# Performance work log

Measured on AMD Instinct MI355X. Metric: run time of the kernel, lower is better.

The kernel has to match this reference:

```python
import jax, jax.numpy as jnp
import numpy as np

H = 64
L = 3
NG = 1024
# node types: 0 user, 1 card, 2 transaction, 3 merchant, 4 location, 5 device
N_NODES = [100000, 150000, 500000, 20000, 5000, 50000]
N_TX = N_NODES[2]
FEAT_DIMS = [8, 6, 12, 6, 5, 5]
NAMES = ["user", "card", "transaction", "merchant", "location", "device"]
# relation r -> (src_type, dst_type); order matches the HeteroConv dict:
# owns, made, at, in, using, followed_by, owned_by, made_with, receives, has, used_in, preceded
REL = [(0, 1), (1, 2), (2, 3), (2, 4), (2, 5), (2, 2), (1, 0), (2, 1), (3, 2), (4, 2), (5, 2), (2, 2)]
E_CNT = [150000, 500000, 500000, 500000, 500000, 500000, 150000, 500000, 500000, 500000, 500000, 500000]


def gat_conv(x_src, x_dst, src, dst, W, a_s, a_d, b, n_dst):
    # PyG GATConv, heads=1, shared src/dst linear (int in_channels), no self-loops (bipartite hetero)
    xs = x_src @ W  # [Ns, H]
    xd = x_dst @ W  # [Nd, H]
    e = jax.nn.leaky_relu((xs @ a_s)[src] + (xd @ a_d)[dst], 0.2)  # [E]
    m = jax.ops.segment_max(e, dst, num_segments=n_dst)
    m = jnp.where(jnp.isfinite(m), m, 0.0)
    p = jnp.exp(e - m[dst])
    s = jax.ops.segment_sum(p, dst, num_segments=n_dst)
    alpha = p / (s[dst] + 1e-16)
    out = jax.ops.segment_sum(alpha[:, None] * xs[src], dst, num_segments=n_dst)
    return out + b


def setup_inputs():
    key = jax.random.key(0)
    ks = iter(jax.random.split(key, 80))
    inp = {}
    for n, d, nm in zip(N_NODES, FEAT_DIMS, NAMES):
        inp["x_" + nm] = jax.random.normal(next(ks), (n, d), jnp.float32)
    for d, nm in zip(FEAT_DIMS, NAMES):
        inp["emb_" + nm + "_W"] = (jax.random.normal(next(ks), (d, H), jnp.float32) / np.sqrt(d)).astype(jnp.float32)
        inp["emb_" + nm + "_b"] = jnp.zeros((H,), jnp.float32)
    inp["gat_W"] = (jax.random.normal(next(ks), (L, 12, H, H), jnp.float32) / np.sqrt(H)).astype(jnp.float32)
    inp["gat_a_src"] = jax.random.normal(next(ks), (L, 12, H), jnp.float32) * 0.1
    inp["gat_a_dst"] = jax.random.normal(next(ks), (L, 12, H), jnp.float32) * 0.1
    inp["gat_b"] = jnp.zeros((L, 12, H), jnp.float32)
    inp["pool_W"] = (jax.random.normal(next(ks), (2 * H, H), jnp.float32) / np.sqrt(2 * H)).astype(jnp.float32)
    inp["pool_b"] = jnp.zeros((H,), jnp.float32)
    inp["cls_W1"] = (jax.random.normal(next(ks), (H, H), jnp.float32) / np.sqrt(H)).astype(jnp.float32)
    inp["cls_b1"] = jnp.zeros((H,), jnp.float32)
    inp["cls_W2"] = (jax.random.normal(next(ks), (H, 1), jnp.float32) / np.sqrt(H)).astype(jnp.float32)
    inp["cls_b2"] = jnp.zeros((1,), jnp.float32)
    for r, (s, d) in enumerate(REL):
        inp[f"e{r}_src"] = jax.random.randint(next(ks), (E_CNT[r],), 0, N_NODES[s])
        inp[f"e{r}_dst"] = jax.random.randint(next(ks), (E_CNT[r],), 0, N_NODES[d])
    inp["batch"] = jnp.sort(jax.random.randint(next(ks), (N_TX,), 0, NG))
    return inp


def reference(x_user, x_card, x_transaction, x_merchant, x_location, x_device,
              emb_user_W, emb_user_b, emb_card_W, emb_card_b,
              emb_transaction_W, emb_transaction_b, emb_merchant_W, emb_merchant_b,
              emb_location_W, emb_location_b, emb_device_W, emb_device_b,
              gat_W, gat_a_src, gat_a_dst, gat_b,
              pool_W, pool_b, cls_W1, cls_b1, cls_W2, cls_b2,
              e0_src, e0_dst, e1_src, e1_dst, e2_src, e2_dst, e3_src, e3_dst,
              e4_src, e4_dst, e5_src, e5_dst, e6_src, e6_dst, e7_src, e7_dst,
              e8_src, e8_dst, e9_src, e9_dst, e10_src, e10_dst, e11_src, e11_dst,
              batch):
    edges = [(e0_src, e0_dst), (e1_src, e1_dst), (e2_src, e2_dst), (e3_src, e3_dst),
             (e4_src, e4_dst), (e5_src, e5_dst), (e6_src, e6_dst), (e7_src, e7_dst),
             (e8_src, e8_dst), (e9_src, e9_dst), (e10_src, e10_dst), (e11_src, e11_dst)]
    x = [x_user @ emb_user_W + emb_user_b,
         x_card @ emb_card_W + emb_card_b,
         x_transaction @ emb_transaction_W + emb_transaction_b,
         x_merchant @ emb_merchant_W + emb_merchant_b,
         x_location @ emb_location_W + emb_location_b,
         x_device @ emb_device_W + emb_device_b]
    for l in range(L):
        agg = [jnp.zeros((n, H), x[0].dtype) for n in N_NODES]
        for r, (s, d) in enumerate(REL):  # HeteroConv default aggr='sum'
            agg[d] = agg[d] + gat_conv(x[s], x[d], edges[r][0], edges[r][1],
                                       gat_W[l, r], gat_a_src[l, r], gat_a_dst[l, r],
                                       gat_b[l, r], N_NODES[d])
        x = [jax.nn.relu(a) for a in agg]  # dropout(p=0.2) is identity in eval mode
    tx = x[2]
    cnt = jax.ops.segment_sum(jnp.ones((N_TX,), tx.dtype), batch, num_segments=NG)
    mean_pool = jax.ops.segment_sum(tx, batch, num_segments=NG) / jnp.maximum(cnt, 1.0)[:, None]
    max_pool = jax.ops.segment_max(tx, batch, num_segments=NG)
    max_pool = jnp.where(jnp.isfinite(max_pool), max_pool, 0.0)
    pooled = jnp.concatenate([mean_pool, max_pool], axis=1) @ pool_W + pool_b
    h = jax.nn.relu(tx @ cls_W1 + cls_b1)
    fraud_scores = jax.nn.sigmoid(h @ cls_W2 + cls_b2)
    return fraud_scores, pooled
```

## Files before the change

### kernel.cpp

```cpp
#include <hip/hip_runtime.h>
#include <hip/hip_bf16.h>

typedef unsigned int u32;
typedef unsigned short u16;
typedef _Float16 f16;
typedef float f32x4 __attribute__((ext_vector_type(4)));
typedef short bf16x8 __attribute__((ext_vector_type(8)));

#define CDIV(a,b) (((a)+(b)-1)/(b))

__device__ __forceinline__ float bf2f(u32 h){ return __uint_as_float(h<<16); }
__device__ __forceinline__ u16 f2bf(float f){
  u32 u=__float_as_uint(f);
  return (u16)((u + 0x7fffu + ((u>>16)&1u))>>16);
}
__device__ __forceinline__ void unpack8(const u16* p, float* xr){
  uint4 v=*(const uint4*)p;
  xr[0]=bf2f(v.x&0xffffu); xr[1]=bf2f(v.x>>16);
  xr[2]=bf2f(v.y&0xffffu); xr[3]=bf2f(v.y>>16);
  xr[4]=bf2f(v.z&0xffffu); xr[5]=bf2f(v.z>>16);
  xr[6]=bf2f(v.w&0xffffu); xr[7]=bf2f(v.w>>16);
}
__device__ __forceinline__ int iclamp(int i, int n){
  unsigned u=(unsigned)i; return (u>=(unsigned)n)?0:i;
}

struct EdgeTab {
  const int* dst[12];
  const int* src[12];
  int seo[13];
  int rpo[13];
  int nd[12];
  int ns[12];
};

struct GTab {
  int nn[6]; int xo[6];
  int rst[12];
  int aso[12], ado[12], rpo[12], seo[12];
  int tord[6]; int bofs[7];
  int abofs[7];
  int nrel[6], rel[6][6];
  int nrole[6]; int rwv[6][12]; int rofs[6][12];
  int dszb;
};

__global__ void kdiag(float* out, int n, float v){
  int i=blockIdx.x*blockDim.x+threadIdx.x;
  if(i<n) out[i]=(i==0)?v:0.f;
}
__global__ void kzeroi(int* p, int n){
  int i=blockIdx.x*blockDim.x+threadIdx.x;
  if(i<n) p[i]=0;
}
__global__ void kbsum(const float* __restrict__ gb, float* __restrict__ bsum){
  int l=blockIdx.x/6, t=blockIdx.x%6, j=threadIdx.x;
  const int rd[12]={1,2,3,4,5,2,0,1,2,2,2,2};
  float a=0.f;
  #pragma unroll
  for(int r=0;r<12;++r) if(rd[r]==t) a += gb[(l*12+r)*64 + j];
  bsum[(l*6+t)*64 + j]=a;
}
__global__ void kwconv(const float* __restrict__ gw, u16* __restrict__ wt, int total){
  int o=blockIdx.x*blockDim.x+threadIdx.x;
  if(o>=total) return;
  int m=o>>12, rem=o&4095, j=rem>>6, k=rem&63;
  wt[o]=f2bf(gw[(m<<12)+(k<<6)+j]);
}
__global__ void kwv(const float* __restrict__ gw, const float* __restrict__ gas,
                    const float* __restrict__ gad, float* __restrict__ wv){
  int m=blockIdx.x;
  int lr=m>>1, role=m&1;
  int k=threadIdx.x;
  const float* a=(role?gad:gas)+(size_t)lr*64;
  const float* W=gw+(size_t)lr*4096;
  float acc=0.f;
  for(int j=0;j<64;++j) acc += W[k*64+j]*a[j];
  wv[(size_t)m*64+k]=acc;
}

__global__ void khistAll(EdgeTab et, int* __restrict__ RP, int Etot){
  int i=blockIdx.x*blockDim.x+threadIdx.x;
  if(i>=Etot) return;
  int r=0;
  #pragma unroll
  for(int k=1;k<12;++k) r += (i>=et.seo[k]) ? 1 : 0;
  int e=i-et.seo[r];
  int d=iclamp(et.dst[r][e], et.nd[r]);
  atomicAdd(RP+et.rpo[r]+d,1);
}
__global__ void kscan1(const int* __restrict__ hist, int* __restrict__ rp, int* __restrict__ bsum, int N){
  __shared__ int lds[256];
  __shared__ int pref[256];
  int b=blockIdx.x, t=threadIdx.x;
  int base=b*4096+t*16;
  int v[16]; int s=0;
  #pragma unroll
  for(int k=0;k<16;++k){ int idx=base+k; v[k]=(idx<N)?hist[idx]:0; s+=v[k]; }
  lds[t]=s; __syncthreads();
  if(t==0){ int run=0; for(int i=0;i<256;++i){ pref[i]=run; run+=lds[i]; } bsum[b]=run; }
  __syncthreads();
  int run=pref[t];
  #pragma unroll
  for(int k=0;k<16;++k){ int idx=base+k; if(idx<N) rp[idx]=run; run+=v[k]; }
}
__global__ void kscan2b(int* bsum, int nb){
  __shared__ int lds[256], pref[256], tot;
  int t=threadIdx.x;
  int v[4]; int s=0;
  #pragma unroll
  for(int k=0;k<4;++k){ int idx=t*4+k; v[k]=(idx<nb)?bsum[idx]:0; s+=v[k]; }
  lds[t]=s; __syncthreads();
  if(t==0){ int run=0; for(int i=0;i<256;++i){ pref[i]=run; run+=lds[i]; } tot=run; }
  __syncthreads();
  int run=pref[t];
  #pragma unroll
  for(int k=0;k<4;++k){ int idx=t*4+k; if(idx<nb){ int x=v[k]; bsum[idx]=run; run+=x; } }
  if(t==0) bsum[nb]=tot;
}
__global__ void kscan3(int* __restrict__ rp, const int* __restrict__ bsum, int N){
  int i=blockIdx.x*blockDim.x+threadIdx.x;
  if(i<N) rp[i]+=bsum[i>>12];
}
__global__ void kscatterAll(EdgeTab et, int* __restrict__ RP, int* __restrict__ SRCS, int Etot){
  int i=blockIdx.x*blockDim.x+threadIdx.x;
  if(i>=Etot) return;
  int r=0;
  #pragma unroll
  for(int k=1;k<12;++k) r += (i>=et.seo[k]) ? 1 : 0;
  int e=i-et.seo[r];
  int d=iclamp(et.dst[r][e], et.nd[r]);
  int pos=atomicAdd(RP+et.rpo[r]+d,1);
  SRCS[pos]=iclamp(et.src[r][e], et.ns[r]);
}

template<int D>
__global__ void kemb(const float* __restrict__ xin, const float* __restrict__ W,
                     const float* __restrict__ b, u16* __restrict__ xout, int N){
  int n=blockIdx.x*blockDim.x+threadIdx.x;
  if(n>=N) return;
  float xr[D];
  #pragma unroll
  for(int k=0;k<D;++k) xr[k]=xin[(long)n*D+k];
  u16* orow=xout+(long)n*64;
  for(int j0=0;j0<64;j0+=8){
    float acc[8];
    #pragma unroll
    for(int jj=0;jj<8;++jj){
      float a=b[j0+jj];
      #pragma unroll
      for(int k=0;k<D;++k) a += xr[k]*W[k*64+j0+jj];
      acc[jj]=a;
    }
    uint4 pk;
    pk.x=(u32)f2bf(acc[0])|((u32)f2bf(acc[1])<<16);
    pk.y=(u32)f2bf(acc[2])|((u32)f2bf(acc[3])<<16);
    pk.z=(u32)f2bf(acc[4])|((u32)f2bf(acc[5])<<16);
    pk.w=(u32)f2bf(acc[6])|((u32)f2bf(acc[7])<<16);
    *(uint4*)(orow+j0)=pk;
  }
}

__global__ void kalphaM(const u16* __restrict__ X, const float* __restrict__ WVl,
                        f16* __restrict__ AA, GTab tab){
  __shared__ float wv[12*64];
  int b=blockIdx.x, tid=threadIdx.x;
  int ti=0;
  #pragma unroll
  for(int k=1;k<6;++k) ti += (b>=tab.abofs[k]) ? 1 : 0;
  int t=tab.tord[ti];
  int nr=tab.nrole[t];
  for(int i=tid;i<nr*64;i+=256){
    int ro=i>>6, j=i&63;
    wv[i]=WVl[tab.rwv[t][ro]*64+j];
  }
  __syncthreads();
  int nid=(b-tab.abofs[ti])*256+tid;
  if(nid>=tab.nn[t]) return;
  const u16* row=X+((long)tab.xo[t]+nid)*64;
  float xr[64];
  #pragma unroll
  for(int j=0;j<64;j+=8) unpack8(row+j,xr+j);
  for(int ro=0;ro<nr;++ro){
    float acc=0.f;
    #pragma unroll
    for(int k=0;k<64;++k) acc += xr[k]*wv[ro*64+k];
    AA[tab.rofs[t][ro]+nid]=(f16)acc;
  }
}

#define LZ 0
#define LW 8192
__global__ void kfusedM2(const u16* __restrict__ Xc, u16* __restrict__ Xn,
                         const u16* __restrict__ WTl, const f16* __restrict__ AA,
                         const int* __restrict__ RP, const int* __restrict__ SRCS,
                         const float* __restrict__ BSl, GTab tab){
  __shared__ char L[16384];
  int tid=threadIdx.x;
  int b=blockIdx.x;
  int ti=0;
  #pragma unroll
  for(int k=1;k<6;++k) ti += (b>=tab.bofs[k]) ? 1 : 0;
  int t=tab.tord[ti];
  int d0=(b-tab.bofs[ti])*64;
  int Nt=tab.nn[t];
  int nid=tid>>2, q=tid&3;
  int d=d0+nid;

  f32x4 acc[4];
  #pragma unroll
  for(int ct=0;ct<4;++ct){ acc[ct][0]=0.f; acc[ct][1]=0.f; acc[ct][2]=0.f; acc[ct][3]=0.f; }

  int nrel=tab.nrel[t];
  for(int ri=0;ri<nrel;++ri){
    int r=tab.rel[t][ri];
    __syncthreads();
    {
      const uint4* s4=(const uint4*)(WTl+(size_t)r*4096);
      uint4 v0=s4[tid*2], v1=s4[tid*2+1];
      int b0=tid*32, j=b0>>7;
      *(uint4*)(L+LW+((b0   )^((j&7)<<4)))=v0;
      *(uint4*)(L+LW+((b0+16)^((j&7)<<4)))=v1;
    }
    float z[16];
    #pragma unroll
    for(int k=0;k<16;++k) z[k]=0.f;
    float sden=0.f;
    if(d<Nt){
      int b1=RP[tab.rpo[r]+d];
      int b0e= d? RP[tab.rpo[r]+d-1] : tab.seo[r];
      float adv=(float)AA[tab.dszb+tab.ado[r]+d];
      const u16* xbase=Xc+(long)tab.xo[tab.rst[r]]*64;
      const f16* asp=AA+tab.aso[r];
      float m=-3.4e38f;
      for(int e=b0e;e<b1;++e){
        float ev=(float)asp[SRCS[e]]+adv;
        ev = ev>=0.f?ev:0.2f*ev;
        m=fmaxf(m,ev);
      }
      int e=b0e;
      for(; e+1<b1; e+=2){
        int sr0=SRCS[e], sr1=SRCS[e+1];
        float ev0=(float)asp[sr0]+adv; ev0 = ev0>=0.f?ev0:0.2f*ev0;
        float ev1=(float)asp[sr1]+adv; ev1 = ev1>=0.f?ev1:0.2f*ev1;
        float p0=__expf(ev0-m), p1=__expf(ev1-m);
        uint4 v0=*(const uint4*)(xbase+(long)sr0*64+q*16);
        uint4 v1=*(const uint4*)(xbase+(long)sr1*64+q*16);
        sden+=p0+p1;
        float xr[8];
        unpack8((const u16*)&v0,xr);
        #pragma unroll
        for(int k=0;k<8;++k) z[k]+=p0*xr[k];
        { uint2 hi; hi.x=v0.z; hi.y=v0.w;
          float xh[4];
          xh[0]=bf2f(hi.x&0xffffu); xh[1]=bf2f(hi.x>>16);
          xh[2]=bf2f(hi.y&0xffffu); xh[3]=bf2f(hi.y>>16);
          (void)xh;
        }
        unpack8((const u16*)&v1,xr);
        #pragma unroll
        for(int k=0;k<8;++k) z[8+k]+=0.f;
        (void)p1;
      }
      #pragma unroll
      for(int k=0;k<16;++k) z[k]=0.f;
      sden=0.f;
      for(e=b0e; e+1<b1; e+=2){
        int sr0=SRCS[e], sr1=SRCS[e+1];
        float ev0=(float)asp[sr0]+adv; ev0 = ev0>=0.f?ev0:0.2f*ev0;
        float ev1=(float)asp[sr1]+adv; ev1 = ev1>=0.f?ev1:0.2f*ev1;
        float p0=__expf(ev0-m), p1=__expf(ev1-m);
        const u16* rw0=xbase+(long)sr0*64+q*16;
        const u16* rw1=xbase+(long)sr1*64+q*16;
        uint4 a0=*(const uint4*)rw0;
        uint4 a1=*(const uint4*)(rw0+8);
        uint4 c0=*(const uint4*)rw1;
        uint4 c1=*(const uint4*)(rw1+8);
        sden+=p0+p1;
        float xr[8];
        unpack8((const u16*)&a0,xr);
        #pragma unroll
        for(int k=0;k<8;++k) z[k]+=p0*xr[k];
        unpack8((const u16*)&a1,xr);
        #pragma unroll
        for(int k=0;k<8;++k) z[8+k]+=p0*xr[k];
        unpack8((const u16*)&c0,xr);
        #pragma unroll
        for(int k=0;k<8;++k) z[k]+=p1*xr[k];
        unpack8((const u16*)&c1,xr);
        #pragma unroll
        for(int k=0;k<8;++k) z[8+k]+=p1*xr[k];
      }
      if(e<b1){
        int sr0=SRCS[e];
        float ev0=(float)asp[sr0]+adv; ev0 = ev0>=0.f?ev0:0.2f*ev0;
        float p0=__expf(ev0-m);
        const u16* rw0=xbase+(long)sr0*64+q*16;
        uint4 a0=*(const uint4*)rw0;
        uint4 a1=*(const uint4*)(rw0+8);
        sden+=p0;
        float xr[8];
        unpack8((const u16*)&a0,xr);
        #pragma unroll
        for(int k=0;k<8;++k) z[k]+=p0*xr[k];
        unpack8((const u16*)&a1,xr);
        #pragma unroll
        for(int k=0;k<8;++k) z[8+k]+=p0*xr[k];
      }
    }
    float inv=1.f/(sden+1e-16f);
    {
      uint4 p0,p1;
      p0.x=(u32)f2bf(z[0]*inv) |((u32)f2bf(z[1]*inv)<<16);
      p0.y=(u32)f2bf(z[2]*inv) |((u32)f2bf(z[3]*inv)<<16);
      p0.z=(u32)f2bf(z[4]*inv) |((u32)f2bf(z[5]*inv)<<16);
      p0.w=(u32)f2bf(z[6]*inv) |((u32)f2bf(z[7]*inv)<<16);
      p1.x=(u32)f2bf(z[8]*inv) |((u32)f2bf(z[9]*inv)<<16);
      p1.y=(u32)f2bf(z[10]*inv)|((u32)f2bf(z[11]*inv)<<16);
      p1.z=(u32)f2bf(z[12]*inv)|((u32)f2bf(z[13]*inv)<<16);
      p1.w=(u32)f2bf(z[14]*inv)|((u32)f2bf(z[15]*inv)<<16);
      int zb=nid*128+q*32;
      *(uint4*)(L+LZ+((zb   )^((nid&7)<<4)))=p0;
      *(uint4*)(L+LZ+((zb+16)^((nid&7)<<4)))=p1;
    }
    __syncthreads();
    {
      int w=tid>>6, l=tid&63;
      int nt=w*16;
      int arow=nt+(l&15);
      int kb=(l>>4)*8;
      #pragma unroll
      for(int ks=0;ks<64;ks+=32){
        int ab=arow*128+(ks+kb)*2;
        uint4 av=*(uint4*)(L+LZ+(ab^((arow&7)<<4)));
        bf16x8 af=*(bf16x8*)&av;
        #pragma unroll
        for(int ct=0;ct<4;++ct){
          int jrow=ct*16+(l&15);
          int bb=jrow*128+(ks+kb)*2;
          uint4 bv=*(uint4*)(L+LW+(bb^((jrow&7)<<4)));
          bf16x8 bfr=*(bf16x8*)&bv;
          acc[ct]=__builtin_amdgcn_mfma_f32_16x16x32_bf16(af,bfr,acc[ct],0,0,0);
        }
      }
    }
  }
  __syncthreads();
  {
    int w=tid>>6, l=tid&63;
    int nt=w*16;
    #pragma unroll
    for(int ct=0;ct<4;++ct){
      #pragma unroll
      for(int r4=0;r4<4;++r4){
        int crow=nt+(l>>4)*4+r4;
        int ccol=ct*16+(l&15);
        int cb=crow*256+ccol*4;
        *(float*)(L+(cb^((crow&7)<<4)))=acc[ct][r4];
      }
    }
  }
  __syncthreads();
  {
    int nn=tid>>2, cq=tid&3;
    if(d0+nn<Nt){
      float cv[16];
      #pragma unroll
      for(int p=0;p<4;++p){
        int cb=nn*256+cq*64+p*16;
        uint4 v=*(uint4*)(L+(cb^((nn&7)<<4)));
        const float* f=(const float*)&v;
        cv[p*4+0]=f[0]; cv[p*4+1]=f[1]; cv[p*4+2]=f[2]; cv[p*4+3]=f[3];
      }
      const float* bs=BSl+t*64+cq*16;
      u32 wd[8];
      #pragma unroll
      for(int i=0;i<8;++i){
        float lo=fmaxf(cv[2*i]  +bs[2*i],  0.f);
        float hi=fmaxf(cv[2*i+1]+bs[2*i+1],0.f);
        wd[i]=(u32)f2bf(lo)|((u32)f2bf(hi)<<16);
      }
      u16* orow=Xn+((long)tab.xo[t]+d0+nn)*64+cq*16;
      uint4 s0; s0.x=wd[0]; s0.y=wd[1]; s0.z=wd[2]; s0.w=wd[3];
      uint4 s1; s1.x=wd[4]; s1.y=wd[5]; s1.z=wd[6]; s1.w=wd[7];
      *(uint4*)orow=s0;
      *(uint4*)(orow+8)=s1;
    }
  }
}

__global__ void kcls(const u16* __restrict__ tx, const float* __restrict__ W1,
                     const float* __restrict__ b1, const float* __restrict__ W2,
                     const float* __restrict__ b2, float* __restrict__ out, int N){
  int n=blockIdx.x*blockDim.x+threadIdx.x;
  if(n>=N) return;
  const u16* row=tx+(long)n*64;
  float xr[64];
  #pragma unroll
  for(int j=0;j<64;j+=8) unpack8(row+j,xr+j);
  float acc2=0.f;
  for(int j=0;j<64;++j){
    float a=b1[j];
    #pragma unroll
    for(int k=0;k<64;++k) a += xr[k]*W1[k*64+j];
    a=fmaxf(a,0.f);
    acc2 += a*W2[j];
  }
  float zv=acc2+b2[0];
  out[n]=1.f/(1.f+__expf(-zv));
}

__global__ void kgrp(const int* __restrict__ batch, int* __restrict__ grp, int N){
  int g=blockIdx.x*blockDim.x+threadIdx.x;
  if(g>1024) return;
  if(g==1024){ grp[1024]=N; return; }
  int lo=0, hi=N;
  while(lo<hi){ int mid=(lo+hi)>>1; if(batch[mid]<g) lo=mid+1; else hi=mid; }
  grp[g]=lo;
}
__global__ void kpoolf(const u16* __restrict__ tx, const int* __restrict__ grp,
                       const float* __restrict__ pW, const float* __restrict__ pb,
                       float* __restrict__ out){
  __shared__ float S[256], M[256], V[128];
  int g=blockIdx.x, t=threadIdx.x, w=t>>6, j=t&63;
  int n0=grp[g], n1=grp[g+1];
  float s=0.f, m=-3.4e38f;
  for(int n=n0+w; n<n1; n+=4){
    float v=bf2f(tx[(long)n*64+j]);
    s+=v; m=fmaxf(m,v);
  }
  S[t]=s; M[t]=m; __syncthreads();
  if(t<64){
    float ss=S[t]+S[t+64]+S[t+128]+S[t+192];
    float mm=fmaxf(fmaxf(M[t],M[t+64]),fmaxf(M[t+128],M[t+192]));
    int cnt=n1-n0;
    V[t]=ss/fmaxf((float)cnt,1.f);
    V[64+t]=(cnt>0)?mm:0.f;
  }
  __syncthreads();
  if(t<64){
    float acc=pb[t];
    for(int k=0;k<128;++k) acc+=V[k]*pW[k*64+t];
    out[(long)g*64+t]=acc;
  }
}

extern "C" void kernel_launch(void* const* d_in, const int* in_sizes, int n_in,
                              void* d_out, int out_size, void* d_ws, size_t ws_size,
                              hipStream_t stream){
  const int   NN[6]={100000,150000,500000,20000,5000,50000};
  const long  XO[6]={0,100000,250000,750000,770000,775000};
  const int   RS[12]={0,1,2,2,2,2,1,2,3,4,5,2};
  const int   RD[12]={1,2,3,4,5,2,0,1,2,2,2,2};
  const int   EC[12]={150000,500000,500000,500000,500000,500000,150000,500000,500000,500000,500000,500000};

  const float* xin[6];  for(int t=0;t<6;++t) xin[t]=(const float*)d_in[t];
  const float* embW[6]; const float* embB[6];
  for(int t=0;t<6;++t){ embW[t]=(const float*)d_in[6+2*t]; embB[t]=(const float*)d_in[7+2*t]; }
  const float* gatW =(const float*)d_in[18];
  const float* gatAs=(const float*)d_in[19];
  const float* gatAd=(const float*)d_in[20];
  const float* gatB =(const float*)d_in[21];
  const float* poolW=(const float*)d_in[22];
  const float* poolB=(const float*)d_in[23];
  const float* W1=(const float*)d_in[24];
  const float* b1=(const float*)d_in[25];
  const float* W2=(const float*)d_in[26];
  const float* b2=(const float*)d_in[27];
  const int* esrc[12]; const int* edst[12];
  for(int r=0;r<12;++r){ esrc[r]=(const int*)d_in[28+2*r]; edst[r]=(const int*)d_in[29+2*r]; }
  const int* batch=(const int*)d_in[52];
  float* out=(float*)d_out;
  (void)in_sizes; (void)n_in;

  EdgeTab et;
  GTab tab;
  int rpo=0, seo=0, asz=0, dsz=0;
  for(int r=0;r<12;++r){
    et.dst[r]=edst[r]; et.src[r]=esrc[r];
    et.seo[r]=seo; et.rpo[r]=rpo;
    et.nd[r]=NN[RD[r]]; et.ns[r]=NN[RS[r]];
    tab.rst[r]=RS[r];
    tab.seo[r]=seo; tab.rpo[r]=rpo;
    tab.aso[r]=asz; tab.ado[r]=dsz;
    seo+=EC[r]; rpo+=NN[RD[r]]+1;
    asz+=NN[RS[r]]; dsz+=NN[RD[r]];
  }
  et.seo[12]=seo; et.rpo[12]=rpo;
  const int Etot=seo;
  const int RPtot=rpo;
  tab.dszb=asz;
  for(int t=0;t<6;++t){ tab.nn[t]=NN[t]; tab.xo[t]=(int)XO[t]; }
  const int TORD[6]={4,3,5,2,1,0};
  int bo=0, abo=0;
  for(int i=0;i<6;++i){
    int t=TORD[i];
    tab.tord[i]=t;
    tab.bofs[i]=bo;   bo+=CDIV(NN[t],64);
    tab.abofs[i]=abo; abo+=CDIV(NN[t],256);
  }
  tab.bofs[6]=bo; tab.abofs[6]=abo;
  for(int t=0;t<6;++t){ tab.nrel[t]=0; tab.nrole[t]=0; }
  for(int r=0;r<12;++r){
    int dt=RD[r];
    tab.rel[dt][tab.nrel[dt]++]=r;
    int st=RS[r];
    tab.rwv[st][tab.nrole[st]]=r*2+0;   tab.rofs[st][tab.nrole[st]++]=tab.aso[r];
    tab.rwv[dt][tab.nrole[dt]]=r*2+1;   tab.rofs[dt][tab.nrole[dt]++]=asz+tab.ado[r];
  }

  char* w=(char*)d_ws;
  size_t off=0;
  auto take=[&](size_t bytes)->void*{
    void* p=w+off; off+=(bytes+(size_t)255)&~(size_t)255; return p;
  };
  u16*   X1   =(u16*)  take(105600000);
  u16*   X2   =(u16*)  take(105600000);
  int*   RP   =(int*)  take((size_t)RPtot*4);
  int*   SRCS =(int*)  take((size_t)Etot*4);
  int*   BS   =(int*)  take(4096);
  f16*   AA   =(f16*)  take((size_t)(asz+dsz)*2);
  float* WV   =(float*)take(72*64*4);
  float* BSUM =(float*)take(4608);
  int*   GRP  =(int*)  take(4104);
  u16*   WT   =(u16*)  take(294912);
  size_t need=off;

  const int B=256;

  if(ws_size<need){
    kdiag<<<CDIV(out_size,B),B,0,stream>>>(out,out_size,(float)(ws_size>>20));
    return;
  }

  int nbs=CDIV(RPtot,4096);
  kzeroi<<<CDIV(RPtot,B),B,0,stream>>>(RP,RPtot);
  khistAll<<<CDIV(Etot,B),B,0,stream>>>(et,RP,Etot);
  kscan1<<<nbs,256,0,stream>>>(RP,RP,BS,RPtot);
  kscan2b<<<1,256,0,stream>>>(BS,nbs);
  kscan3<<<CDIV(RPtot,B),B,0,stream>>>(RP,BS,RPtot);
  kscatterAll<<<CDIV(Etot,B),B,0,stream>>>(et,RP,SRCS,Etot);

  kwconv<<<CDIV(147456,B),B,0,stream>>>(gatW,WT,147456);
  kwv<<<72,64,0,stream>>>(gatW,gatAs,gatAd,WV);
  kbsum<<<18,64,0,stream>>>(gatB,BSUM);

  kemb< 8><<<CDIV(NN[0],B),B,0,stream>>>(xin[0],embW[0],embB[0],X1+XO[0]*64,NN[0]);
  kemb< 6><<<CDIV(NN[1],B),B,0,stream>>>(xin[1],embW[1],embB[1],X1+XO[1]*64,NN[1]);
  kemb<12><<<CDIV(NN[2],B),B,0,stream>>>(xin[2],embW[2],embB[2],X1+XO[2]*64,NN[2]);
  kemb< 6><<<CDIV(NN[3],B),B,0,stream>>>(xin[3],embW[3],embB[3],X1+XO[3]*64,NN[3]);
  kemb< 5><<<CDIV(NN[4],B),B,0,stream>>>(xin[4],embW[4],embB[4],X1+XO[4]*64,NN[4]);
  kemb< 5><<<CDIV(NN[5],B),B,0,stream>>>(xin[5],embW[5],embB[5],X1+XO[5]*64,NN[5]);

  u16* Xc=X1; u16* Xn=X2;
  for(int l=0;l<3;++l){
    kalphaM<<<abo,256,0,stream>>>(Xc,WV+(size_t)l*1536,AA,tab);
    kfusedM2<<<bo,256,0,stream>>>(Xc,Xn,WT+(size_t)l*49152,AA,RP,SRCS,BSUM+(size_t)l*384,tab);
    u16* tmp=Xc; Xc=Xn; Xn=tmp;
  }

  kcls<<<CDIV(NN[2],B),B,0,stream>>>(Xc+XO[2]*64,W1,b1,W2,b2,out,NN[2]);

  kgrp<<<CDIV(1025,B),B,0,stream>>>(batch,GRP,NN[2]);
  kpoolf<<<1024,256,0,stream>>>(Xc+XO[2]*64,GRP,poolW,poolB,out+500000);
}
```

Baseline: 2.491 ms.

## Chunk CSR build, fuse layer-0 attention logits into embedding, drop dead loop

Splits the destination histogram and scatter into 8 passes, each over a range of row-pointer indices, so the atomics in one pass stay within a smaller region and may get better cache locality. The cost is reading all edges 8 times per pass. Folds the layer-0 attention logit computation into the embedding kernel and skips the separate kalphaM launch for layer 0. Removes a leftover first aggregation loop in the fused conv kernel whose results were thrown away, which wasted gathers and exps.

```diff
diff --git a/kernel.cpp b/kernel.cpp
--- a/kernel.cpp
+++ b/kernel.cpp
@@ -79,15 +79,15 @@
   wv[(size_t)m*64+k]=acc;
 }
 
-__global__ void khistAll(EdgeTab et, int* __restrict__ RP, int Etot){
+__global__ void khistC(EdgeTab et, int* __restrict__ RP, int Etot, int c0, int c1){
   int i=blockIdx.x*blockDim.x+threadIdx.x;
   if(i>=Etot) return;
   int r=0;
   #pragma unroll
   for(int k=1;k<12;++k) r += (i>=et.seo[k]) ? 1 : 0;
   int e=i-et.seo[r];
-  int d=iclamp(et.dst[r][e], et.nd[r]);
-  atomicAdd(RP+et.rpo[r]+d,1);
+  int rpidx=et.rpo[r]+iclamp(et.dst[r][e], et.nd[r]);
+  if(rpidx>=c0 && rpidx<c1) atomicAdd(RP+rpidx,1);
 }
 __global__ void kscan1(const int* __restrict__ hist, int* __restrict__ rp, int* __restrict__ bsum, int N){
   __shared__ int lds[256];
@@ -122,42 +122,55 @@
   int i=blockIdx.x*blockDim.x+threadIdx.x;
   if(i<N) rp[i]+=bsum[i>>12];
 }
-__global__ void kscatterAll(EdgeTab et, int* __restrict__ RP, int* __restrict__ SRCS, int Etot){
+__global__ void kscatterC(EdgeTab et, int* __restrict__ RP, int* __restrict__ SRCS,
+                          int Etot, int c0, int c1){
   int i=blockIdx.x*blockDim.x+threadIdx.x;
   if(i>=Etot) return;
   int r=0;
   #pragma unroll
   for(int k=1;k<12;++k) r += (i>=et.seo[k]) ? 1 : 0;
   int e=i-et.seo[r];
-  int d=iclamp(et.dst[r][e], et.nd[r]);
-  int pos=atomicAdd(RP+et.rpo[r]+d,1);
-  SRCS[pos]=iclamp(et.src[r][e], et.ns[r]);
+  int rpidx=et.rpo[r]+iclamp(et.dst[r][e], et.nd[r]);
+  if(rpidx>=c0 && rpidx<c1){
+    int pos=atomicAdd(RP+rpidx,1);
+    SRCS[pos]=iclamp(et.src[r][e], et.ns[r]);
+  }
 }
 
 template<int D>
 __global__ void kemb(const float* __restrict__ xin, const float* __restrict__ W,
-                     const float* __restrict__ b, u16* __restrict__ xout, int N){
+                     const float* __restrict__ b, u16* __restrict__ xout, int N,
+                     const float* __restrict__ WV0, f16* __restrict__ AA, GTab tab, int t){
   int n=blockIdx.x*blockDim.x+threadIdx.x;
   if(n>=N) return;
   float xr[D];
   #pragma unroll
   for(int k=0;k<D;++k) xr[k]=xin[(long)n*D+k];
+  float o[64];
   u16* orow=xout+(long)n*64;
+  #pragma unroll
   for(int j0=0;j0<64;j0+=8){
-    float acc[8];
     #pragma unroll
     for(int jj=0;jj<8;++jj){
       float a=b[j0+jj];
       #pragma unroll
       for(int k=0;k<D;++k) a += xr[k]*W[k*64+j0+jj];
-      acc[jj]=a;
+      o[j0+jj]=a;
     }
     uint4 pk;
-    pk.x=(u32)f2bf(acc[0])|((u32)f2bf(acc[1])<<16);
-    pk.y=(u32)f2bf(acc[2])|((u32)f2bf(acc[3])<<16);
-    pk.z=(u32)f2bf(acc[4])|((u32)f2bf(acc[5])<<16);
-    pk.w=(u32)f2bf(acc[6])|((u32)f2bf(acc[7])<<16);
+    pk.x=(u32)f2bf(o[j0+0])|((u32)f2bf(o[j0+1])<<16);
+    pk.y=(u32)f2bf(o[j0+2])|((u32)f2bf(o[j0+3])<<16);
+    pk.z=(u32)f2bf(o[j0+4])|((u32)f2bf(o[j0+5])<<16);
+    pk.w=(u32)f2bf(o[j0+6])|((u32)f2bf(o[j0+7])<<16);
     *(uint4*)(orow+j0)=pk;
+  }
+  int nr=tab.nrole[t];
+  for(int ro=0;ro<nr;++ro){
+    const float* wv=WV0+(size_t)tab.rwv[t][ro]*64;
+    float acc=0.f;
+    #pragma unroll
+    for(int k=0;k<64;++k) acc += o[k]*wv[k];
+    AA[tab.rofs[t][ro]+n]=(f16)acc;
   }
 }
 
@@ -240,32 +253,6 @@
       }
       int e=b0e;
       for(; e+1<b1; e+=2){
-        int sr0=SRCS[e], sr1=SRCS[e+1];
-        float ev0=(float)asp[sr0]+adv; ev0 = ev0>=0.f?ev0:0.2f*ev0;
-        float ev1=(float)asp[sr1]+adv; ev1 = ev1>=0.f?ev1:0.2f*ev1;
-        float p0=__expf(ev0-m), p1=__expf(ev1-m);
-        uint4 v0=*(const uint4*)(xbase+(long)sr0*64+q*16);
-        uint4 v1=*(const uint4*)(xbase+(long)sr1*64+q*16);
-        sden+=p0+p1;
-        float xr[8];
-        unpack8((const u16*)&v0,xr);
-        #pragma unroll
-        for(int k=0;k<8;++k) z[k]+=p0*xr[k];
-        { uint2 hi; hi.x=v0.z; hi.y=v0.w;
-          float xh[4];
-          xh[0]=bf2f(hi.x&0xffffu); xh[1]=bf2f(hi.x>>16);
-          xh[2]=bf2f(hi.y&0xffffu); xh[3]=bf2f(hi.y>>16);
-          (void)xh;
-        }
-        unpack8((const u16*)&v1,xr);
-        #pragma unroll
-        for(int k=0;k<8;++k) z[8+k]+=0.f;
-        (void)p1;
-      }
-      #pragma unroll
-      for(int k=0;k<16;++k) z[k]=0.f;
-      sden=0.f;
-      for(e=b0e; e+1<b1; e+=2){
         int sr0=SRCS[e], sr1=SRCS[e+1];
         float ev0=(float)asp[sr0]+adv; ev0 = ev0>=0.f?ev0:0.2f*ev0;
         float ev1=(float)asp[sr1]+adv; ev1 = ev1>=0.f?ev1:0.2f*ev1;
@@ -533,29 +520,38 @@
     return;
   }
 
+  kwconv<<<CDIV(147456,B),B,0,stream>>>(gatW,WT,147456);
+  kwv<<<72,64,0,stream>>>(gatW,gatAs,gatAd,WV);
+  kbsum<<<18,64,0,stream>>>(gatB,BSUM);
+
+  const int NCH=8;
+  int CS=CDIV(RPtot,NCH);
+  kzeroi<<<CDIV(RPtot,B),B,0,stream>>>(RP,RPtot);
+  for(int c=0;c<NCH;++c){
+    int c0=c*CS, c1=min(RPtot,c0+CS);
+    khistC<<<CDIV(Etot,B),B,0,stream>>>(et,RP,Etot,c0,c1);
+  }
   int nbs=CDIV(RPtot,4096);
-  kzeroi<<<CDIV(RPtot,B),B,0,stream>>>(RP,RPtot);
-  khistAll<<<CDIV(Etot,B),B,0,stream>>>(et,RP,Etot);
   kscan1<<<nbs,256,0,stream>>>(RP,RP,BS,RPtot);
   kscan2b<<<1,256,0,stream>>>(BS,nbs);
   kscan3<<<CDIV(RPtot,B),B,0,stream>>>(RP,BS,RPtot);
-  kscatterAll<<<CDIV(Etot,B),B,0,stream>>>(et,RP,SRCS,Etot);
-
-  kwconv<<<CDIV(147456,B),B,0,stream>>>(gatW,WT,147456);
-  kwv<<<72,64,0,stream>>>(gatW,gatAs,gatAd,WV);
-  kbsum<<<18,64,0,stream>>>(gatB,BSUM);
-
-  kemb< 8><<<CDIV(NN[0],B),B,0,stream>>>(xin[0],embW[0],embB[0],X1+XO[0]*64,NN[0]);
-  kemb< 6><<<CDIV(NN[1],B),B,0,stream>>>(xin[1],embW[1],embB[1],X1+XO[1]*64,NN[1]);
-  kemb<12><<<CDIV(NN[2],B),B,0,stream>>>(xin[2],embW[2],embB[2],X1+XO[2]*64,NN[2]);
-  kemb< 6><<<CDIV(NN[3],B),B,0,stream>>>(xin[3],embW[3],embB[3],X1+XO[3]*64,NN[3]);
-  kemb< 5><<<CDIV(NN[4],B),B,0,stream>>>(xin[4],embW[4],embB[4],X1+XO[4]*64,NN[4]);
-  kemb< 5><<<CDIV(NN[5],B),B,0,stream>>>(xin[5],embW[5],embB[5],X1+XO[5]*64,NN[5]);
+  for(int c=0;c<NCH;++c){
+    int c0=c*CS, c1=min(RPtot,c0+CS);
+    kscatterC<<<CDIV(Etot,B),B,0,stream>>>(et,RP,SRCS,Etot,c0,c1);
+  }
+
+  kemb< 8><<<CDIV(NN[0],B),B,0,stream>>>(xin[0],embW[0],embB[0],X1+XO[0]*64,NN[0],WV,AA,tab,0);
+  kemb< 6><<<CDIV(NN[1],B),B,0,stream>>>(xin[1],embW[1],embB[1],X1+XO[1]*64,NN[1],WV,AA,tab,1);
+  kemb<12><<<CDIV(NN[2],B),B,0,stream>>>(xin[2],embW[2],embB[2],X1+XO[2]*64,NN[2],WV,AA,tab,2);
+  kemb< 6><<<CDIV(NN[3],B),B,0,stream>>>(xin[3],embW[3],embB[3],X1+XO[3]*64,NN[3],WV,AA,tab,3);
+  kemb< 5><<<CDIV(NN[4],B),B,0,stream>>>(xin[4],embW[4],embB[4],X1+XO[4]*64,NN[4],WV,AA,tab,4);
+  kemb< 5><<<CDIV(NN[5],B),B,0,stream>>>(xin[5],embW[5],embB[5],X1+XO[5]*64,NN[5],WV,AA,tab,5);
 
   u16* Xc=X1; u16* Xn=X2;
   for(int l=0;l<3;++l){
-    kalphaM<<<abo,256,0,stream>>>(Xc,WV+(size_t)l*1536,AA,tab);
-    kfusedM2<<<bo,256,0,stream>>>(Xc,Xn,WT+(size_t)l*49152,AA,RP,SRCS,BSUM+(size_t)l*384,tab);
+    if(l>0) kalphaM<<<abo,256,0,stream>>>(Xc,WV+(size_t)l*1536,AA,tab);
+    kfusedM2<<<bo,256,0,stream>>>(Xc,Xn,WT+(size_t)l*49152,AA,RP,SRCS,
+                                  BSUM+(size_t)l*384,tab);
     u16* tmp=Xc; Xc=Xn; Xn=tmp;
   }
 
```

Measured after the change: 2.506 ms. Within noise of the previous version (+0.6%).
